# Optimization experiments

Hardware: AMD Instinct MI355X
Metric: run time of the kernel (lower is better)

## Reference

```python
import jax, jax.numpy as jnp
import numpy as np

N_NODES = 8192
RANK = 5
HIDDEN = 128
BATCH = 8
DT = 0.1
N_STEPS = 10  # round(total_time / dt) = round(1.0 / 0.1)


def setup_inputs() -> dict:
    key = jax.random.key(0)
    ks = jax.random.split(key, 16)
    s_in = 1.0 / np.sqrt(N_NODES)
    s_h = 1.0 / np.sqrt(HIDDEN)
    return {
        "x0": jax.random.uniform(ks[0], (BATCH, N_NODES), jnp.float32),
        "Ls": jax.random.normal(ks[1], (N_NODES, N_NODES), jnp.float32),
        "Lf": jax.random.normal(ks[2], (N_NODES, N_NODES), jnp.float32),
        # GatedInitializer MLP (stored as [in, out] so forward is x @ W + b)
        "W1": jax.random.uniform(ks[3], (N_NODES, HIDDEN), jnp.float32, -s_in, s_in),
        "b1": jnp.zeros((HIDDEN,), jnp.float32),
        "W2": jax.random.uniform(ks[4], (HIDDEN, N_NODES), jnp.float32, -s_h, s_h),
        "b2": jnp.zeros((N_NODES,), jnp.float32),
        # low-rank coupling factors
        "Ms_A": 0.05 * jax.random.normal(ks[5], (N_NODES, RANK), jnp.float32),
        "Ms_B": 0.05 * jax.random.normal(ks[6], (N_NODES, RANK), jnp.float32),
        "Mf_A": 0.05 * jax.random.normal(ks[7], (N_NODES, RANK), jnp.float32),
        "Mf_B": 0.05 * jax.random.normal(ks[8], (N_NODES, RANK), jnp.float32),
        "raw_cs": jnp.float32(0.0),
        "raw_cf": jnp.float32(0.0),
        "raw_lambda_s": jnp.float32(-1.0),
        "raw_lambda_f": jnp.float32(-1.0),
        # decoder MLP
        "D1": jax.random.uniform(ks[9], (N_NODES, HIDDEN), jnp.float32, -s_in, s_in),
        "db1": jnp.zeros((HIDDEN,), jnp.float32),
        "D2": jax.random.uniform(ks[10], (HIDDEN, N_NODES), jnp.float32, -s_h, s_h),
        "db2": jnp.zeros((N_NODES,), jnp.float32),
    }


def reference(x0, Ls, Lf, W1, b1, W2, b2, Ms_A, Ms_B, Mf_A, Mf_B,
              raw_cs, raw_cf, raw_lambda_s, raw_lambda_f, D1, db1, D2, db2):
    # gated split of initial signal
    gate = jax.nn.sigmoid(jax.nn.relu(x0 @ W1 + b1) @ W2 + b2)  # [B, N]
    us = gate * x0
    uf = (1.0 - gate) * x0

    eps = jnp.float32(1e-4)
    c_s = jax.nn.softplus(raw_cs) + eps
    c_f = jax.nn.softplus(raw_cf) + eps
    l_s = jax.nn.softplus(raw_lambda_s) + eps
    l_f = jax.nn.softplus(raw_lambda_f) + eps

    Ms = Ms_A @ Ms_B.T  # [N, N] low-rank coupling
    Mf = Mf_A @ Mf_B.T

    dt = jnp.float32(DT)

    def step(carry, _):
        us, uf = carry
        dus = -c_s * (us @ Ls.T) + l_s * (uf @ Ms.T)
        duf = -c_f * (uf @ Lf.T) + l_f * (us @ Mf.T)
        us = jnp.maximum(us + dt * dus, 0.0)
        uf = jnp.maximum(uf + dt * duf, 0.0)
        return (us, uf), None

    (us, uf), _ = jax.lax.scan(step, (us, uf), None, length=N_STEPS)

    latent_sum = us + uf
    x1_hat = jax.nn.softplus(jax.nn.relu(latent_sum @ D1 + db1) @ D2 + db2)
    return (x1_hat, us, uf)
```

## Files before the change

kernel.cpp:

```cpp
#include <hip/hip_runtime.h>
#include <hip/hip_bf16.h>
#include <math.h>

#define N     8192
#define NB    8
#define HID   128
#define RANK  5
#define DT    0.1f
#define JC    2048

__device__ __forceinline__ float softplusf(float x) {
    return fmaxf(x, 0.0f) + log1pf(expf(-fabsf(x)));
}

__global__ void mlp1_partial(const float* __restrict__ in0,
                             const float* __restrict__ in1,
                             const float* __restrict__ W,
                             float* __restrict__ partial,
                             int add_two)
{
    __shared__ float xs[NB][128];
    const int kb = blockIdx.x;
    const int j  = threadIdx.x;
    for (int t = threadIdx.x; t < NB * 128; t += 128) {
        int b = t >> 7, kk = t & 127;
        int k = kb * 128 + kk;
        float v = in0[(size_t)b * N + k];
        if (add_two) v += in1[(size_t)b * N + k];
        xs[b][kk] = v;
    }
    __syncthreads();
    float acc[NB];
#pragma unroll
    for (int b = 0; b < NB; ++b) acc[b] = 0.f;
    for (int kk = 0; kk < 128; ++kk) {
        float w = W[(size_t)(kb * 128 + kk) * HID + j];
#pragma unroll
        for (int b = 0; b < NB; ++b) acc[b] = fmaf(xs[b][kk], w, acc[b]);
    }
#pragma unroll
    for (int b = 0; b < NB; ++b) partial[(size_t)(kb * NB + b) * HID + j] = acc[b];
}

__global__ void mlp1_reduce(const float* __restrict__ partial,
                            const float* __restrict__ bias,
                            float* __restrict__ h)
{
    int b = blockIdx.x, j = threadIdx.x;
    float s = bias[j];
    for (int kb = 0; kb < 64; ++kb) s += partial[(size_t)(kb * NB + b) * HID + j];
    h[b * HID + j] = fmaxf(s, 0.f);
}

__global__ void mlp2_gate(const float* __restrict__ h, const float* __restrict__ W2,
                          const float* __restrict__ b2, const float* __restrict__ x0,
                          float* __restrict__ us, float* __restrict__ uf)
{
    __shared__ float hs[NB][HID];
    for (int t = threadIdx.x; t < NB * HID; t += 128) hs[t >> 7][t & 127] = h[t];
    __syncthreads();
    int i = blockIdx.x * 128 + threadIdx.x;
    float bb = b2[i];
    float acc[NB];
#pragma unroll
    for (int b = 0; b < NB; ++b) acc[b] = bb;
    for (int jj = 0; jj < HID; ++jj) {
        float w = W2[(size_t)jj * N + i];
#pragma unroll
        for (int b = 0; b < NB; ++b) acc[b] = fmaf(hs[b][jj], w, acc[b]);
    }
#pragma unroll
    for (int b = 0; b < NB; ++b) {
        float g = 1.f / (1.f + expf(-acc[b]));
        float x = x0[(size_t)b * N + i];
        us[(size_t)b * N + i] = g * x;
        uf[(size_t)b * N + i] = (1.f - g) * x;
    }
}

__global__ void mlp2_dec(const float* __restrict__ h, const float* __restrict__ W2,
                         const float* __restrict__ b2, float* __restrict__ out)
{
    __shared__ float hs[NB][HID];
    for (int t = threadIdx.x; t < NB * HID; t += 128) hs[t >> 7][t & 127] = h[t];
    __syncthreads();
    int i = blockIdx.x * 128 + threadIdx.x;
    float bb = b2[i];
    float acc[NB];
#pragma unroll
    for (int b = 0; b < NB; ++b) acc[b] = bb;
    for (int jj = 0; jj < HID; ++jj) {
        float w = W2[(size_t)jj * N + i];
#pragma unroll
        for (int b = 0; b < NB; ++b) acc[b] = fmaf(hs[b][jj], w, acc[b]);
    }
#pragma unroll
    for (int b = 0; b < NB; ++b) out[(size_t)b * N + i] = softplusf(acc[b]);
}

__global__ void pk(const float* __restrict__ us, const float* __restrict__ uf,
                   const float* __restrict__ MsB, const float* __restrict__ MfB,
                   float* __restrict__ p)
{
    __shared__ float red[256];
    const int m = blockIdx.x / 40, rem = blockIdx.x % 40;
    const int b = rem / RANK, r = rem % RANK;
    const float* u  = m ? us : uf;
    const float* Bm = m ? MfB : MsB;
    float s = 0.f;
    for (int j = threadIdx.x; j < N; j += 256)
        s += u[(size_t)b * N + j] * Bm[(size_t)j * RANK + r];
    red[threadIdx.x] = s;
    __syncthreads();
    for (int w = 128; w > 0; w >>= 1) {
        if (threadIdx.x < w) red[threadIdx.x] += red[threadIdx.x + w];
        __syncthreads();
    }
    if (threadIdx.x == 0) p[m * 40 + rem] = red[0];
}

__global__ __launch_bounds__(256, 2) void step_kernel(
    const float* __restrict__ us_in, const float* __restrict__ uf_in,
    float* __restrict__ us_out, float* __restrict__ uf_out,
    const float* __restrict__ Ls, const float* __restrict__ Lf,
    const float* __restrict__ MsA, const float* __restrict__ MfA,
    const float* __restrict__ p,
    const float* __restrict__ rcs, const float* __restrict__ rcf,
    const float* __restrict__ rls, const float* __restrict__ rlf)
{
    __shared__ float u_lds[NB][JC];
    const int bid  = blockIdx.x;
    const bool isf = bid >= 256;
    const int row0 = (bid & 255) * 32;
    const int wave = threadIdx.x >> 6;
    const int lane = threadIdx.x & 63;
    const float* __restrict__ u_in = isf ? uf_in : us_in;
    const float* __restrict__ L    = isf ? Lf : Ls;
    const int rowbase = row0 + wave * 8;

    float acc[8][NB];
#pragma unroll
    for (int r = 0; r < 8; ++r)
#pragma unroll
        for (int b = 0; b < NB; ++b) acc[r][b] = 0.f;

    for (int chunk = 0; chunk < N / JC; ++chunk) {
        const int jbase = chunk * JC;
        __syncthreads();
        for (int t = threadIdx.x; t < NB * JC / 4; t += 256) {
            int flat = t * 4;
            int b = flat / JC, jj = flat % JC;
            *(float4*)&u_lds[b][jj] = *(const float4*)&u_in[(size_t)b * N + jbase + jj];
        }
        __syncthreads();
        for (int jit = 0; jit < JC / 256; ++jit) {
            const int jl = jit * 256 + lane * 4;
            float4 uv[NB];
#pragma unroll
            for (int b = 0; b < NB; ++b) uv[b] = *(const float4*)&u_lds[b][jl];
#pragma unroll
            for (int r = 0; r < 8; ++r) {
                const float4 a = *(const float4*)&L[(size_t)(rowbase + r) * N + jbase + jl];
#pragma unroll
                for (int b = 0; b < NB; ++b) {
                    acc[r][b] = fmaf(a.x, uv[b].x, acc[r][b]);
                    acc[r][b] = fmaf(a.y, uv[b].y, acc[r][b]);
                    acc[r][b] = fmaf(a.z, uv[b].z, acc[r][b]);
                    acc[r][b] = fmaf(a.w, uv[b].w, acc[r][b]);
                }
            }
        }
    }

    __syncthreads();
    float* red = &u_lds[0][0];
#pragma unroll
    for (int r = 0; r < 8; ++r)
#pragma unroll
        for (int b = 0; b < NB; ++b)
            red[(size_t)(wave * 64 + r * 8 + b) * 64 + lane] = acc[r][b];
    __syncthreads();

    {
        const int tid = threadIdx.x;
        const int w = tid >> 6, v = tid & 63;
        const int r = v >> 3, b = v & 7;
        const float* base = red + (size_t)tid * 64;
        float s = 0.f;
#pragma unroll
        for (int i = 0; i < 64; ++i) s += base[(v + i) & 63];

        const int row = row0 + w * 8 + r;
        if (!isf) {
            float c = softplusf(rcs[0]) + 1e-4f;
            float l = softplusf(rls[0]) + 1e-4f;
            float lr = 0.f;
#pragma unroll
            for (int rr = 0; rr < RANK; ++rr)
                lr = fmaf(p[b * RANK + rr], MsA[(size_t)row * RANK + rr], lr);
            float v0 = us_in[(size_t)b * N + row];
            float du = fmaf(-c, s, l * lr);
            us_out[(size_t)b * N + row] = fmaxf(fmaf(DT, du, v0), 0.f);
        } else {
            float c = softplusf(rcf[0]) + 1e-4f;
            float l = softplusf(rlf[0]) + 1e-4f;
            float lr = 0.f;
#pragma unroll
            for (int rr = 0; rr < RANK; ++rr)
                lr = fmaf(p[40 + b * RANK + rr], MfA[(size_t)row * RANK + rr], lr);
            float v0 = uf_in[(size_t)b * N + row];
            float du = fmaf(-c, s, l * lr);
            uf_out[(size_t)b * N + row] = fmaxf(fmaf(DT, du, v0), 0.f);
        }
    }
}

extern "C" void kernel_launch(void* const* d_in, const int* in_sizes, int n_in,
                              void* d_out, int out_size, void* d_ws, size_t ws_size,
                              hipStream_t stream) {
    const float* x0  = (const float*)d_in[0];
    const float* Ls  = (const float*)d_in[1];
    const float* Lf  = (const float*)d_in[2];
    const float* W1  = (const float*)d_in[3];
    const float* b1  = (const float*)d_in[4];
    const float* W2  = (const float*)d_in[5];
    const float* b2  = (const float*)d_in[6];
    const float* MsA = (const float*)d_in[7];
    const float* MsB = (const float*)d_in[8];
    const float* MfA = (const float*)d_in[9];
    const float* MfB = (const float*)d_in[10];
    const float* rcs = (const float*)d_in[11];
    const float* rcf = (const float*)d_in[12];
    const float* rls = (const float*)d_in[13];
    const float* rlf = (const float*)d_in[14];
    const float* D1  = (const float*)d_in[15];
    const float* db1 = (const float*)d_in[16];
    const float* D2  = (const float*)d_in[17];
    const float* db2 = (const float*)d_in[18];

    float* out = (float*)d_out;
    float* ws  = (float*)d_ws;

    float* usA = ws;
    float* ufA = ws + 65536;
    float* usB = ws + 131072;
    float* ufB = ws + 196608;
    float* p   = ws + 262144;
    float* h   = ws + 262400;
    float* prt = ws + 263424;

    mlp1_partial<<<64, 128, 0, stream>>>(x0, x0, W1, prt, 0);
    mlp1_reduce<<<8, 128, 0, stream>>>(prt, b1, h);
    mlp2_gate<<<64, 128, 0, stream>>>(h, W2, b2, x0, usA, ufA);

    float *ui = usA, *vi = ufA, *uo = usB, *vo = ufB;
    for (int t = 0; t < 10; ++t) {
        pk<<<80, 256, 0, stream>>>(ui, vi, MsB, MfB, p);
        float* uso = (t == 9) ? (out + 65536)  : uo;
        float* ufo = (t == 9) ? (out + 131072) : vo;
        step_kernel<<<512, 256, 0, stream>>>(ui, vi, uso, ufo, Ls, Lf, MsA, MfA, p,
                                             rcs, rcf, rls, rlf);
        float* tmp;
        tmp = ui; ui = uo; uo = tmp;
        tmp = vi; vi = vo; vo = tmp;
    }

    mlp1_partial<<<64, 128, 0, stream>>>(out + 65536, out + 131072, D1, prt, 1);
    mlp1_reduce<<<8, 128, 0, stream>>>(prt, db1, h);
    mlp2_dec<<<64, 128, 0, stream>>>(h, D2, db2, out);
}
```

Baseline: 1.307 ms.

## Drop LDS staging in step kernel, halve rows per block, use shuffle reduction

The step kernel now reads the state vectors directly from global memory instead of staging 2048-wide chunks in shared memory. Each wave handles 4 rows instead of 8, the grid doubles to 1024 blocks and the launch bound targets 4 blocks per CU. The cross-lane reduction now uses a register butterfly of xor shuffles instead of an LDS transpose. The aim is higher occupancy and no block-wide barriers while streaming the large L matrices, at the cost of re-reading u from cache in every block.

```diff
diff --git a/kernel.cpp b/kernel.cpp
--- a/kernel.cpp
+++ b/kernel.cpp
@@ -7,7 +7,6 @@
 #define HID   128
 #define RANK  5
 #define DT    0.1f
-#define JC    2048
 
 __device__ __forceinline__ float softplusf(float x) {
     return fmaxf(x, 0.0f) + log1pf(expf(-fabsf(x)));
@@ -119,7 +118,7 @@
     if (threadIdx.x == 0) p[m * 40 + rem] = red[0];
 }
 
-__global__ __launch_bounds__(256, 2) void step_kernel(
+__global__ __launch_bounds__(256, 4) void step_kernel(
     const float* __restrict__ us_in, const float* __restrict__ uf_in,
     float* __restrict__ us_out, float* __restrict__ uf_out,
     const float* __restrict__ Ls, const float* __restrict__ Lf,
@@ -128,69 +127,55 @@
     const float* __restrict__ rcs, const float* __restrict__ rcf,
     const float* __restrict__ rls, const float* __restrict__ rlf)
 {
-    __shared__ float u_lds[NB][JC];
     const int bid  = blockIdx.x;
-    const bool isf = bid >= 256;
-    const int row0 = (bid & 255) * 32;
+    const bool isf = bid >= 512;
+    const int row0 = (bid & 511) * 16;
     const int wave = threadIdx.x >> 6;
     const int lane = threadIdx.x & 63;
     const float* __restrict__ u_in = isf ? uf_in : us_in;
     const float* __restrict__ L    = isf ? Lf : Ls;
-    const int rowbase = row0 + wave * 8;
-
-    float acc[8][NB];
-#pragma unroll
-    for (int r = 0; r < 8; ++r)
-#pragma unroll
-        for (int b = 0; b < NB; ++b) acc[r][b] = 0.f;
-
-    for (int chunk = 0; chunk < N / JC; ++chunk) {
-        const int jbase = chunk * JC;
-        __syncthreads();
-        for (int t = threadIdx.x; t < NB * JC / 4; t += 256) {
-            int flat = t * 4;
-            int b = flat / JC, jj = flat % JC;
-            *(float4*)&u_lds[b][jj] = *(const float4*)&u_in[(size_t)b * N + jbase + jj];
-        }
-        __syncthreads();
-        for (int jit = 0; jit < JC / 256; ++jit) {
-            const int jl = jit * 256 + lane * 4;
-            float4 uv[NB];
-#pragma unroll
-            for (int b = 0; b < NB; ++b) uv[b] = *(const float4*)&u_lds[b][jl];
-#pragma unroll
-            for (int r = 0; r < 8; ++r) {
-                const float4 a = *(const float4*)&L[(size_t)(rowbase + r) * N + jbase + jl];
-#pragma unroll
-                for (int b = 0; b < NB; ++b) {
-                    acc[r][b] = fmaf(a.x, uv[b].x, acc[r][b]);
-                    acc[r][b] = fmaf(a.y, uv[b].y, acc[r][b]);
-                    acc[r][b] = fmaf(a.z, uv[b].z, acc[r][b]);
-                    acc[r][b] = fmaf(a.w, uv[b].w, acc[r][b]);
-                }
+    const int rowbase = row0 + wave * 4;
+
+    float acc[32];
+#pragma unroll
+    for (int i = 0; i < 32; ++i) acc[i] = 0.f;
+
+    for (int jit = 0; jit < N / 256; ++jit) {
+        const int j = jit * 256 + lane * 4;
+        float4 uv[NB];
+#pragma unroll
+        for (int b = 0; b < NB; ++b) uv[b] = *(const float4*)&u_in[(size_t)b * N + j];
+#pragma unroll
+        for (int r = 0; r < 4; ++r) {
+            const float4 a = *(const float4*)&L[(size_t)(rowbase + r) * N + j];
+#pragma unroll
+            for (int b = 0; b < NB; ++b) {
+                acc[r * 8 + b] = fmaf(a.x, uv[b].x, acc[r * 8 + b]);
+                acc[r * 8 + b] = fmaf(a.y, uv[b].y, acc[r * 8 + b]);
+                acc[r * 8 + b] = fmaf(a.z, uv[b].z, acc[r * 8 + b]);
+                acc[r * 8 + b] = fmaf(a.w, uv[b].w, acc[r * 8 + b]);
             }
         }
     }
 
-    __syncthreads();
-    float* red = &u_lds[0][0];
-#pragma unroll
-    for (int r = 0; r < 8; ++r)
-#pragma unroll
-        for (int b = 0; b < NB; ++b)
-            red[(size_t)(wave * 64 + r * 8 + b) * 64 + lane] = acc[r][b];
-    __syncthreads();
-
-    {
-        const int tid = threadIdx.x;
-        const int w = tid >> 6, v = tid & 63;
+#pragma unroll
+    for (int m = 32; m >= 2; m >>= 1) {
+        const bool hi = (lane & m) != 0;
+        const int half = m >> 1;
+#pragma unroll
+        for (int i = 0; i < half; ++i) {
+            float send = hi ? acc[i] : acc[i + half];
+            float recv = __shfl_xor(send, m, 64);
+            acc[i] = (hi ? acc[i + half] : acc[i]) + recv;
+        }
+    }
+    acc[0] += __shfl_xor(acc[0], 1, 64);
+
+    if ((lane & 1) == 0) {
+        const int v = lane >> 1;
         const int r = v >> 3, b = v & 7;
-        const float* base = red + (size_t)tid * 64;
-        float s = 0.f;
-#pragma unroll
-        for (int i = 0; i < 64; ++i) s += base[(v + i) & 63];
-
-        const int row = row0 + w * 8 + r;
+        const int row = rowbase + r;
+        const float s = acc[0];
         if (!isf) {
             float c = softplusf(rcs[0]) + 1e-4f;
             float l = softplusf(rls[0]) + 1e-4f;
@@ -258,8 +243,8 @@
         pk<<<80, 256, 0, stream>>>(ui, vi, MsB, MfB, p);
         float* uso = (t == 9) ? (out + 65536)  : uo;
         float* ufo = (t == 9) ? (out + 131072) : vo;
-        step_kernel<<<512, 256, 0, stream>>>(ui, vi, uso, ufo, Ls, Lf, MsA, MfA, p,
-                                             rcs, rcf, rls, rlf);
+        step_kernel<<<1024, 256, 0, stream>>>(ui, vi, uso, ufo, Ls, Lf, MsA, MfA, p,
+                                              rcs, rcf, rls, rlf);
         float* tmp;
         tmp = ui; ui = uo; uo = tmp;
         tmp = vi; vi = vo; vo = tmp;
@@ -267,5 +252,5 @@
 
     mlp1_partial<<<64, 128, 0, stream>>>(out + 65536, out + 131072, D1, prt, 1);
     mlp1_reduce<<<8, 128, 0, stream>>>(prt, db1, h);
-    mlp2_dec<<<64, 128, 0, stream>>>(h, D2, db2, out);
-}
+    mlp2_dec<<<8 * 8, 128, 0, stream>>>(h, D2, db2, out);
+}
```

After: 1.505 ms. 1.15x slower.
